# Optimization experiments

Hardware: AMD Instinct MI355X
Metric: run time of the kernel (lower is better)

Reference implementation:

```python
import jax, jax.numpy as jnp
import numpy as np

B, T, C, H = 4, 2048, 768, 12
D = C // H  # head dim = 64

def setup_inputs() -> dict:
    key = jax.random.key(0)
    k1, k2, k3 = jax.random.split(key, 3)
    x = jax.random.normal(k1, (B, T, C), dtype=jnp.float32)
    W_attn = jax.random.normal(k2, (C, 3 * C), dtype=jnp.float32) * 0.02
    b_attn = jnp.zeros((3 * C,), dtype=jnp.float32)
    W_proj = jax.random.normal(k3, (C, C), dtype=jnp.float32) * 0.02
    b_proj = jnp.zeros((C,), dtype=jnp.float32)
    return {"x": x, "W_attn": W_attn, "b_attn": b_attn, "W_proj": W_proj, "b_proj": b_proj}

def reference(x, W_attn, b_attn, W_proj, b_proj):
    Bx, Tx, Cx = x.shape
    qkv = x @ W_attn + b_attn                      # [B,T,3C]
    q, k, v = jnp.split(qkv, 3, axis=2)
    q = q.reshape(Bx, Tx, H, D).swapaxes(1, 2)     # [B,H,T,D]
    k = k.reshape(Bx, Tx, H, D).swapaxes(1, 2)
    v = v.reshape(Bx, Tx, H, D).swapaxes(1, 2)
    att = jnp.einsum('bhqd,bhkd->bhqk', q, k) / jnp.sqrt(jnp.float32(D))
    mask = jnp.tril(jnp.ones((Tx, Tx), dtype=bool))
    att = jnp.where(mask, att, -jnp.inf)
    att = jax.nn.softmax(att, axis=-1)
    y = jnp.einsum('bhqk,bhkd->bhqd', att, v)      # [B,H,T,D]
    y = y.swapaxes(1, 2).reshape(Bx, Tx, Cx)
    return y @ W_proj + b_proj
```

## Files before the change

### kernel.cpp

```cpp
#include <hip/hip_runtime.h>
#include <hip/hip_bf16.h>

#define BATCH 4
#define TSEQ  2048
#define CDIM  768
#define HNUM  12
#define DHEAD 64
#define NQKV  (3*CDIM)
#define BTOT  (BATCH*TSEQ)
#define BH    (BATCH*HNUM)

typedef unsigned short u16;
typedef __attribute__((ext_vector_type(8))) __bf16 bf16x8;
typedef __attribute__((ext_vector_type(4))) float f32x4;

#define MFMA16(a,b,c) __builtin_amdgcn_mfma_f32_16x16x32_bf16((a),(b),(c),0,0,0)

__device__ __forceinline__ u16 f2b(float f) {
    union { float f; unsigned u; } v; v.f = f;
    unsigned u = v.u;
    unsigned r = (u + 0x7fffu + ((u >> 16) & 1u)) >> 16;
    return (u16)r;
}

__device__ __forceinline__ unsigned cvtpk(float lo, float hi) {
    unsigned r;
    asm("v_cvt_pk_bf16_f32 %0, %1, %2" : "=v"(r) : "v"(lo), "v"(hi));
    return r;
}

__device__ __forceinline__ float fexp2(float x) {
    float r;
    asm("v_exp_f32 %0, %1" : "=v"(r) : "v"(x));
    return r;
}

__device__ __forceinline__ void gload_lds(const void* g, void* l) {
    __builtin_amdgcn_global_load_lds(
        (const __attribute__((address_space(1))) void*)g,
        (__attribute__((address_space(3))) void*)l, 16, 0, 0);
}

__global__ __launch_bounds__(256) void cast_f32_bf16(
        const float* __restrict__ in, u16* __restrict__ out, int n4) {
    int i = blockIdx.x * blockDim.x + threadIdx.x;
    if (i >= n4) return;
    float4 a = reinterpret_cast<const float4*>(in)[i];
    ushort4 o;
    o.x = f2b(a.x); o.y = f2b(a.y); o.z = f2b(a.z); o.w = f2b(a.w);
    reinterpret_cast<ushort4*>(out)[i] = o;
}

__global__ __launch_bounds__(256) void tcast(
        const float* __restrict__ in, u16* __restrict__ out, int R, int Cc) {
    __shared__ float tile[32][33];
    int c0 = blockIdx.x * 32, r0 = blockIdx.y * 32;
    int tx = threadIdx.x, ty = threadIdx.y;
    #pragma unroll
    for (int i = 0; i < 32; i += 8)
        tile[ty + i][tx] = in[(size_t)(r0 + ty + i) * Cc + c0 + tx];
    __syncthreads();
    #pragma unroll
    for (int i = 0; i < 32; i += 8)
        out[(size_t)(c0 + ty + i) * R + r0 + tx] = f2b(tile[tx][ty + i]);
}

template<int MODE>
__global__ __launch_bounds__(256) void gemm_bt(
        const u16* __restrict__ A, const u16* __restrict__ Bt,
        const float* __restrict__ bias,
        u16* __restrict__ qb, u16* __restrict__ kb, u16* __restrict__ vtb,
        float* __restrict__ outf, int M, int N, int K) {
    __shared__ u16 sA[2][128 * 32];
    __shared__ u16 sB[2][128 * 32];
    const int tid = threadIdx.x;
    const int lane = tid & 63;
    const int w = tid >> 6;
    const int wr = w >> 1, wc = w & 1;
    const int m0 = blockIdx.y * 128, n0 = blockIdx.x * 128;

    f32x4 acc[4][4] = {};

    auto stage = [&](int buf, int kt) {
        #pragma unroll
        for (int i = 0; i < 2; ++i) {
            int chunk = i * 256 + tid;
            int row = chunk >> 2, c8 = chunk & 3;
            gload_lds(A  + (size_t)(m0 + row) * K + kt * 32 + c8 * 8, &sA[buf][chunk * 8]);
            gload_lds(Bt + (size_t)(n0 + row) * K + kt * 32 + c8 * 8, &sB[buf][chunk * 8]);
        }
    };

    const int KT = K / 32;
    stage(0, 0);
    __syncthreads();
    for (int kt = 0; kt < KT; ++kt) {
        if (kt + 1 < KT) stage((kt + 1) & 1, kt + 1);
        const u16* cA = sA[kt & 1];
        const u16* cB = sB[kt & 1];
        bf16x8 af[4], bfr[4];
        #pragma unroll
        for (int m = 0; m < 4; ++m)
            af[m] = *(const bf16x8*)&cA[(wr * 64 + m * 16 + (lane & 15)) * 32 + ((lane >> 4) << 3)];
        #pragma unroll
        for (int n = 0; n < 4; ++n)
            bfr[n] = *(const bf16x8*)&cB[(wc * 64 + n * 16 + (lane & 15)) * 32 + ((lane >> 4) << 3)];
        #pragma unroll
        for (int m = 0; m < 4; ++m)
            #pragma unroll
            for (int n = 0; n < 4; ++n)
                acc[m][n] = MFMA16(af[m], bfr[n], acc[m][n]);
        __syncthreads();
    }

    if (MODE == 0) {
        const int which = n0 / CDIM;
        #pragma unroll
        for (int m = 0; m < 4; ++m) {
            #pragma unroll
            for (int n = 0; n < 4; ++n) {
                const int cg = n0 + wc * 64 + n * 16 + (lane & 15);
                const int c  = cg - which * CDIM;
                const int h  = c >> 6, d = c & 63;
                const float bv = bias[cg];
                const int rg0 = m0 + wr * 64 + m * 16 + ((lane >> 4) << 2);
                const int b = rg0 >> 11, t0 = rg0 & (TSEQ - 1);
                const size_t bh = (size_t)(b * HNUM + h);
                if (which == 2) {
                    ushort4 pv;
                    pv.x = f2b(acc[m][n][0] + bv);
                    pv.y = f2b(acc[m][n][1] + bv);
                    pv.z = f2b(acc[m][n][2] + bv);
                    pv.w = f2b(acc[m][n][3] + bv);
                    *(ushort4*)&vtb[(bh * DHEAD + d) * TSEQ + t0] = pv;
                } else {
                    #pragma unroll
                    for (int j = 0; j < 4; ++j) {
                        const float val = acc[m][n][j] + bv;
                        if (which == 0) qb[(bh * TSEQ + t0 + j) * DHEAD + d] = f2b(val * 0.1803368801111243f);
                        else            kb[(bh * TSEQ + t0 + j) * DHEAD + d] = f2b(val);
                    }
                }
            }
        }
    } else {
        #pragma unroll
        for (int m = 0; m < 4; ++m) {
            #pragma unroll
            for (int n = 0; n < 4; ++n) {
                const int cg = n0 + wc * 64 + n * 16 + (lane & 15);
                const float bv = bias[cg];
                #pragma unroll
                for (int j = 0; j < 4; ++j) {
                    const int rg = m0 + wr * 64 + m * 16 + ((lane >> 4) << 2) + j;
                    outf[(size_t)rg * CDIM + cg] = acc[m][n][j] + bv;
                }
            }
        }
    }
}

__global__ __launch_bounds__(512, 4) void attn_fwd(
        const u16* __restrict__ qb, const u16* __restrict__ kb,
        const u16* __restrict__ vtb, u16* __restrict__ yb) {
    __shared__ u16 sK[2][64 * 64];
    __shared__ u16 sVt[2][64 * 64];
    const int p  = blockIdx.x / BH;
    const int bh = blockIdx.x % BH;
    const int b = bh / HNUM, h = bh % HNUM;
    const int tid = threadIdx.x, lane = tid & 63, w = tid >> 6;
    const int g = lane >> 4, lq = lane & 15;
    const int qtile = (w < 4) ? p : (31 - p);
    const int qlo = qtile * 64 + (w & 3) * 16;
    const u16* qbase = qb  + (size_t)bh * TSEQ * DHEAD;
    const u16* kbase = kb  + (size_t)bh * TSEQ * DHEAD;
    const u16* vbase = vtb + (size_t)bh * DHEAD * TSEQ;

    bf16x8 qf[2];
    #pragma unroll
    for (int ks = 0; ks < 2; ++ks)
        qf[ks] = *(const bf16x8*)&qbase[(size_t)(qlo + lq) * DHEAD + ks * 32 + g * 8];

    f32x4 o[4] = {};
    float mx = -__builtin_inff(), ls = 0.f;

    const int srow = tid >> 3;
    const int lcol = (((tid & 7) << 4) ^ ((srow & 7) << 4)) >> 1;

    auto STAGE = [&](int buf, int kt) {
        const int k0 = kt << 6;
        gload_lds(kbase + (size_t)(k0 + srow) * DHEAD + lcol, &sK[buf][tid * 8]);
        gload_lds(vbase + (size_t)srow * TSEQ + k0 + lcol,    &sVt[buf][tid * 8]);
    };

    const int nk = 32 - p;
    STAGE(0, 0);
    __syncthreads();
    for (int kt = 0; kt < nk; ++kt) {
        const int k0 = kt << 6;
        if (kt + 1 < nk) STAGE((kt + 1) & 1, kt + 1);
        if (k0 <= qlo + 15) {
            const u16* cK = sK[kt & 1];
            const u16* cV = sVt[kt & 1];
            f32x4 s[4];
            #pragma unroll
            for (int n = 0; n < 4; ++n) s[n] = f32x4{0.f, 0.f, 0.f, 0.f};
            __builtin_amdgcn_s_setprio(1);
            #pragma unroll
            for (int n = 0; n < 4; ++n) {
                #pragma unroll
                for (int ks = 0; ks < 2; ++ks) {
                    int r = n * 16 + lq;
                    int lb = (r * 128 + (ks * 32 + g * 8) * 2) ^ ((r & 7) << 4);
                    bf16x8 kf = *(const bf16x8*)((const char*)cK + lb);
                    s[n] = MFMA16(kf, qf[ks], s[n]);
                }
            }
            __builtin_amdgcn_s_setprio(0);
            if (k0 + 63 > qlo) {
                const int qa = qlo + lq;
                #pragma unroll
                for (int n = 0; n < 4; ++n)
                    #pragma unroll
                    for (int j = 0; j < 4; ++j)
                        if (k0 + n * 16 + g * 4 + j > qa) s[n][j] = -__builtin_inff();
            }
            float t0 = fmaxf(fmaxf(s[0][0], s[0][1]), fmaxf(s[0][2], s[0][3]));
            float t1 = fmaxf(fmaxf(s[1][0], s[1][1]), fmaxf(s[1][2], s[1][3]));
            float t2 = fmaxf(fmaxf(s[2][0], s[2][1]), fmaxf(s[2][2], s[2][3]));
            float t3 = fmaxf(fmaxf(s[3][0], s[3][1]), fmaxf(s[3][2], s[3][3]));
            float tmax = fmaxf(fmaxf(t0, t1), fmaxf(t2, t3));
            tmax = fmaxf(tmax, __shfl_xor(tmax, 16));
            tmax = fmaxf(tmax, __shfl_xor(tmax, 32));
            if (__any(tmax > mx + 8.0f)) {
                float mnew = fmaxf(mx, tmax);
                float sc = fexp2(mx - mnew);
                mx = mnew;
                ls *= sc;
                #pragma unroll
                for (int j = 0; j < 4; ++j) {
                    float scj = __shfl(sc, (lane & 48) | ((g << 2) + j));
                    #pragma unroll
                    for (int n = 0; n < 4; ++n) o[n][j] *= scj;
                }
            }
            float rsum = 0.f;
            #pragma unroll
            for (int n = 0; n < 4; ++n)
                #pragma unroll
                for (int j = 0; j < 4; ++j) {
                    float pv = fexp2(s[n][j] - mx);
                    s[n][j] = pv;
                    rsum += pv;
                }
            rsum += __shfl_xor(rsum, 16);
            rsum += __shfl_xor(rsum, 32);
            ls += rsum;
            unsigned apk[4], bpk[4];
            #pragma unroll
            for (int n = 0; n < 4; ++n) {
                apk[n] = cvtpk(s[n][0], s[n][1]);
                bpk[n] = cvtpk(s[n][2], s[n][3]);
            }
            const int s0l = lq + ((lane & 16) << 1);
            const bool hi = (lane & 32) != 0;
            #pragma unroll
            for (int ks = 0; ks < 2; ++ks) {
                unsigned A0  = (unsigned)__shfl((int)apk[2 * ks],     s0l);
                unsigned B0  = (unsigned)__shfl((int)bpk[2 * ks],     s0l);
                unsigned A1  = (unsigned)__shfl((int)apk[2 * ks + 1], s0l);
                unsigned B1  = (unsigned)__shfl((int)bpk[2 * ks + 1], s0l);
                unsigned A0h = (unsigned)__shfl((int)apk[2 * ks],     s0l + 16);
                unsigned B0h = (unsigned)__shfl((int)bpk[2 * ks],     s0l + 16);
                unsigned A1h = (unsigned)__shfl((int)apk[2 * ks + 1], s0l + 16);
                unsigned B1h = (unsigned)__shfl((int)bpk[2 * ks + 1], s0l + 16);
                union { unsigned u[4]; bf16x8 v; } pa;
                pa.u[0] = hi ? A1  : A0;
                pa.u[1] = hi ? B1  : B0;
                pa.u[2] = hi ? A1h : A0h;
                pa.u[3] = hi ? B1h : B0h;
                __builtin_amdgcn_s_setprio(1);
                #pragma unroll
                for (int n = 0; n < 4; ++n) {
                    int d = n * 16 + lq;
                    int lb = (d * 128 + (ks * 32 + g * 8) * 2) ^ ((d & 7) << 4);
                    bf16x8 vf = *(const bf16x8*)((const char*)cV + lb);
                    o[n] = MFMA16(pa.v, vf, o[n]);
                }
                __builtin_amdgcn_s_setprio(0);
            }
        }
        __syncthreads();
    }

    #pragma unroll
    for (int j = 0; j < 4; ++j) {
        float lj = __shfl(ls, (lane & 48) | ((g << 2) + j));
        float inv = 1.f / lj;
        const int t = qlo + g * 4 + j;
        #pragma unroll
        for (int n = 0; n < 4; ++n) {
            const int c = h * DHEAD + n * 16 + lq;
            yb[((size_t)b * TSEQ + t) * CDIM + c] = f2b(o[n][j] * inv);
        }
    }
}

extern "C" void kernel_launch(void* const* d_in, const int* in_sizes, int n_in,
                              void* d_out, int out_size, void* d_ws, size_t ws_size,
                              hipStream_t stream) {
    const float* x      = (const float*)d_in[0];
    const float* W_attn = (const float*)d_in[1];
    const float* b_attn = (const float*)d_in[2];
    const float* W_proj = (const float*)d_in[3];
    const float* b_proj = (const float*)d_in[4];
    float* out = (float*)d_out;

    u16* ws = (u16*)d_ws;
    u16* xb     = ws;
    u16* yb     = xb;
    u16* WattnT = xb     + (size_t)BTOT * CDIM;
    u16* WprojT = WattnT + (size_t)NQKV * CDIM;
    u16* qb     = WprojT + (size_t)CDIM * CDIM;
    u16* kb     = qb     + (size_t)BH * TSEQ * DHEAD;
    u16* vtb    = kb     + (size_t)BH * TSEQ * DHEAD;

    int n4 = BTOT * CDIM / 4;
    cast_f32_bf16<<<(n4 + 255) / 256, 256, 0, stream>>>(x, xb, n4);
    tcast<<<dim3(NQKV / 32, CDIM / 32), dim3(32, 8), 0, stream>>>(W_attn, WattnT, CDIM, NQKV);
    tcast<<<dim3(CDIM / 32, CDIM / 32), dim3(32, 8), 0, stream>>>(W_proj, WprojT, CDIM, CDIM);

    gemm_bt<0><<<dim3(NQKV / 128, BTOT / 128), 256, 0, stream>>>(
        xb, WattnT, b_attn, qb, kb, vtb, nullptr, BTOT, NQKV, CDIM);

    attn_fwd<<<dim3((TSEQ / 128) * BH), 512, 0, stream>>>(qb, kb, vtb, yb);

    gemm_bt<1><<<dim3(CDIM / 128, BTOT / 128), 256, 0, stream>>>(
        yb, WprojT, b_proj, nullptr, nullptr, nullptr, out, BTOT, CDIM, CDIM);
}
```

Baseline: 166.9 us.

## Use one 64-row query tile per attention block and compute row sums via MFMA

Attention blocks shrink from 512 threads covering a paired short and long query tile to 256 threads covering a single 64-row tile. Blocks are ordered longest-first, and since the tile is diagonal-aligned every wave runs every key tile, so the per-wave causal skip branch is gone. The softmax denominator is now accumulated with an extra MFMA against a ones vector, replacing the shuffle reductions and the final broadcast. The cost is twice as many blocks, each staging two chunks per thread, and K/V tiles are no longer shared across two query tiles.

```diff
diff --git a/kernel.cpp b/kernel.cpp
--- a/kernel.cpp
+++ b/kernel.cpp
@@ -160,18 +160,17 @@
     }
 }
 
-__global__ __launch_bounds__(512, 4) void attn_fwd(
+__global__ __launch_bounds__(256, 4) void attn_fwd(
         const u16* __restrict__ qb, const u16* __restrict__ kb,
         const u16* __restrict__ vtb, u16* __restrict__ yb) {
     __shared__ u16 sK[2][64 * 64];
     __shared__ u16 sVt[2][64 * 64];
-    const int p  = blockIdx.x / BH;
+    const int qt = 31 - (int)(blockIdx.x / BH);
     const int bh = blockIdx.x % BH;
     const int b = bh / HNUM, h = bh % HNUM;
     const int tid = threadIdx.x, lane = tid & 63, w = tid >> 6;
     const int g = lane >> 4, lq = lane & 15;
-    const int qtile = (w < 4) ? p : (31 - p);
-    const int qlo = qtile * 64 + (w & 3) * 16;
+    const int qlo = qt * 64 + w * 16;
     const u16* qbase = qb  + (size_t)bh * TSEQ * DHEAD;
     const u16* kbase = kb  + (size_t)bh * TSEQ * DHEAD;
     const u16* vbase = vtb + (size_t)bh * DHEAD * TSEQ;
@@ -181,122 +180,121 @@
     for (int ks = 0; ks < 2; ++ks)
         qf[ks] = *(const bf16x8*)&qbase[(size_t)(qlo + lq) * DHEAD + ks * 32 + g * 8];
 
+    union { unsigned u[4]; bf16x8 v; } ones;
+    #pragma unroll
+    for (int i = 0; i < 4; ++i) ones.u[i] = 0x3f803f80u;
+
     f32x4 o[4] = {};
-    float mx = -__builtin_inff(), ls = 0.f;
-
-    const int srow = tid >> 3;
-    const int lcol = (((tid & 7) << 4) ^ ((srow & 7) << 4)) >> 1;
+    f32x4 ls = {};
+    float mx = -__builtin_inff();
 
     auto STAGE = [&](int buf, int kt) {
         const int k0 = kt << 6;
-        gload_lds(kbase + (size_t)(k0 + srow) * DHEAD + lcol, &sK[buf][tid * 8]);
-        gload_lds(vbase + (size_t)srow * TSEQ + k0 + lcol,    &sVt[buf][tid * 8]);
+        #pragma unroll
+        for (int i = 0; i < 2; ++i) {
+            int chunk = i * 256 + tid;
+            int srow = chunk >> 3;
+            int cb = ((chunk & 7) << 4) ^ ((srow & 7) << 4);
+            gload_lds(kbase + (size_t)(k0 + srow) * DHEAD + (cb >> 1), &sK[buf][chunk * 8]);
+            gload_lds(vbase + (size_t)srow * TSEQ + k0 + (cb >> 1),    &sVt[buf][chunk * 8]);
+        }
     };
 
-    const int nk = 32 - p;
+    const int nk = qt + 1;
     STAGE(0, 0);
     __syncthreads();
     for (int kt = 0; kt < nk; ++kt) {
         const int k0 = kt << 6;
         if (kt + 1 < nk) STAGE((kt + 1) & 1, kt + 1);
-        if (k0 <= qlo + 15) {
-            const u16* cK = sK[kt & 1];
-            const u16* cV = sVt[kt & 1];
-            f32x4 s[4];
-            #pragma unroll
-            for (int n = 0; n < 4; ++n) s[n] = f32x4{0.f, 0.f, 0.f, 0.f};
-            __builtin_amdgcn_s_setprio(1);
-            #pragma unroll
-            for (int n = 0; n < 4; ++n) {
-                #pragma unroll
-                for (int ks = 0; ks < 2; ++ks) {
-                    int r = n * 16 + lq;
-                    int lb = (r * 128 + (ks * 32 + g * 8) * 2) ^ ((r & 7) << 4);
-                    bf16x8 kf = *(const bf16x8*)((const char*)cK + lb);
-                    s[n] = MFMA16(kf, qf[ks], s[n]);
-                }
-            }
-            __builtin_amdgcn_s_setprio(0);
-            if (k0 + 63 > qlo) {
-                const int qa = qlo + lq;
-                #pragma unroll
-                for (int n = 0; n < 4; ++n)
-                    #pragma unroll
-                    for (int j = 0; j < 4; ++j)
-                        if (k0 + n * 16 + g * 4 + j > qa) s[n][j] = -__builtin_inff();
-            }
-            float t0 = fmaxf(fmaxf(s[0][0], s[0][1]), fmaxf(s[0][2], s[0][3]));
-            float t1 = fmaxf(fmaxf(s[1][0], s[1][1]), fmaxf(s[1][2], s[1][3]));
-            float t2 = fmaxf(fmaxf(s[2][0], s[2][1]), fmaxf(s[2][2], s[2][3]));
-            float t3 = fmaxf(fmaxf(s[3][0], s[3][1]), fmaxf(s[3][2], s[3][3]));
-            float tmax = fmaxf(fmaxf(t0, t1), fmaxf(t2, t3));
-            tmax = fmaxf(tmax, __shfl_xor(tmax, 16));
-            tmax = fmaxf(tmax, __shfl_xor(tmax, 32));
-            if (__any(tmax > mx + 8.0f)) {
-                float mnew = fmaxf(mx, tmax);
-                float sc = fexp2(mx - mnew);
-                mx = mnew;
-                ls *= sc;
-                #pragma unroll
-                for (int j = 0; j < 4; ++j) {
-                    float scj = __shfl(sc, (lane & 48) | ((g << 2) + j));
-                    #pragma unroll
-                    for (int n = 0; n < 4; ++n) o[n][j] *= scj;
-                }
-            }
-            float rsum = 0.f;
+        const u16* cK = sK[kt & 1];
+        const u16* cV = sVt[kt & 1];
+        f32x4 s[4];
+        #pragma unroll
+        for (int n = 0; n < 4; ++n) s[n] = f32x4{0.f, 0.f, 0.f, 0.f};
+        __builtin_amdgcn_s_setprio(1);
+        #pragma unroll
+        for (int n = 0; n < 4; ++n) {
+            #pragma unroll
+            for (int ks = 0; ks < 2; ++ks) {
+                int r = n * 16 + lq;
+                int lb = (r * 128 + (ks * 32 + g * 8) * 2) ^ ((r & 7) << 4);
+                bf16x8 kf = *(const bf16x8*)((const char*)cK + lb);
+                s[n] = MFMA16(kf, qf[ks], s[n]);
+            }
+        }
+        __builtin_amdgcn_s_setprio(0);
+        if (k0 + 63 > qlo) {
+            const int qa = qlo + lq;
             #pragma unroll
             for (int n = 0; n < 4; ++n)
                 #pragma unroll
-                for (int j = 0; j < 4; ++j) {
-                    float pv = fexp2(s[n][j] - mx);
-                    s[n][j] = pv;
-                    rsum += pv;
-                }
-            rsum += __shfl_xor(rsum, 16);
-            rsum += __shfl_xor(rsum, 32);
-            ls += rsum;
-            unsigned apk[4], bpk[4];
+                for (int j = 0; j < 4; ++j)
+                    if (k0 + n * 16 + g * 4 + j > qa) s[n][j] = -__builtin_inff();
+        }
+        float t0 = fmaxf(fmaxf(s[0][0], s[0][1]), fmaxf(s[0][2], s[0][3]));
+        float t1 = fmaxf(fmaxf(s[1][0], s[1][1]), fmaxf(s[1][2], s[1][3]));
+        float t2 = fmaxf(fmaxf(s[2][0], s[2][1]), fmaxf(s[2][2], s[2][3]));
+        float t3 = fmaxf(fmaxf(s[3][0], s[3][1]), fmaxf(s[3][2], s[3][3]));
+        float tmax = fmaxf(fmaxf(t0, t1), fmaxf(t2, t3));
+        tmax = fmaxf(tmax, __shfl_xor(tmax, 16));
+        tmax = fmaxf(tmax, __shfl_xor(tmax, 32));
+        if (__any(tmax > mx + 8.0f)) {
+            float mnew = fmaxf(mx, tmax);
+            float sc = fexp2(mx - mnew);
+            mx = mnew;
+            #pragma unroll
+            for (int j = 0; j < 4; ++j) {
+                float scj = __shfl(sc, (lane & 48) | ((g << 2) + j));
+                ls[j] *= scj;
+                #pragma unroll
+                for (int n = 0; n < 4; ++n) o[n][j] *= scj;
+            }
+        }
+        #pragma unroll
+        for (int n = 0; n < 4; ++n)
+            #pragma unroll
+            for (int j = 0; j < 4; ++j)
+                s[n][j] = fexp2(s[n][j] - mx);
+        unsigned apk[4], bpk[4];
+        #pragma unroll
+        for (int n = 0; n < 4; ++n) {
+            apk[n] = cvtpk(s[n][0], s[n][1]);
+            bpk[n] = cvtpk(s[n][2], s[n][3]);
+        }
+        const int s0l = lq + ((lane & 16) << 1);
+        const bool hi = (lane & 32) != 0;
+        #pragma unroll
+        for (int ks = 0; ks < 2; ++ks) {
+            unsigned A0  = (unsigned)__shfl((int)apk[2 * ks],     s0l);
+            unsigned B0  = (unsigned)__shfl((int)bpk[2 * ks],     s0l);
+            unsigned A1  = (unsigned)__shfl((int)apk[2 * ks + 1], s0l);
+            unsigned B1  = (unsigned)__shfl((int)bpk[2 * ks + 1], s0l);
+            unsigned A0h = (unsigned)__shfl((int)apk[2 * ks],     s0l + 16);
+            unsigned B0h = (unsigned)__shfl((int)bpk[2 * ks],     s0l + 16);
+            unsigned A1h = (unsigned)__shfl((int)apk[2 * ks + 1], s0l + 16);
+            unsigned B1h = (unsigned)__shfl((int)bpk[2 * ks + 1], s0l + 16);
+            union { unsigned u[4]; bf16x8 v; } pa;
+            pa.u[0] = hi ? A1  : A0;
+            pa.u[1] = hi ? B1  : B0;
+            pa.u[2] = hi ? A1h : A0h;
+            pa.u[3] = hi ? B1h : B0h;
+            __builtin_amdgcn_s_setprio(1);
             #pragma unroll
             for (int n = 0; n < 4; ++n) {
-                apk[n] = cvtpk(s[n][0], s[n][1]);
-                bpk[n] = cvtpk(s[n][2], s[n][3]);
-            }
-            const int s0l = lq + ((lane & 16) << 1);
-            const bool hi = (lane & 32) != 0;
-            #pragma unroll
-            for (int ks = 0; ks < 2; ++ks) {
-                unsigned A0  = (unsigned)__shfl((int)apk[2 * ks],     s0l);
-                unsigned B0  = (unsigned)__shfl((int)bpk[2 * ks],     s0l);
-                unsigned A1  = (unsigned)__shfl((int)apk[2 * ks + 1], s0l);
-                unsigned B1  = (unsigned)__shfl((int)bpk[2 * ks + 1], s0l);
-                unsigned A0h = (unsigned)__shfl((int)apk[2 * ks],     s0l + 16);
-                unsigned B0h = (unsigned)__shfl((int)bpk[2 * ks],     s0l + 16);
-                unsigned A1h = (unsigned)__shfl((int)apk[2 * ks + 1], s0l + 16);
-                unsigned B1h = (unsigned)__shfl((int)bpk[2 * ks + 1], s0l + 16);
-                union { unsigned u[4]; bf16x8 v; } pa;
-                pa.u[0] = hi ? A1  : A0;
-                pa.u[1] = hi ? B1  : B0;
-                pa.u[2] = hi ? A1h : A0h;
-                pa.u[3] = hi ? B1h : B0h;
-                __builtin_amdgcn_s_setprio(1);
-                #pragma unroll
-                for (int n = 0; n < 4; ++n) {
-                    int d = n * 16 + lq;
-                    int lb = (d * 128 + (ks * 32 + g * 8) * 2) ^ ((d & 7) << 4);
-                    bf16x8 vf = *(const bf16x8*)((const char*)cV + lb);
-                    o[n] = MFMA16(pa.v, vf, o[n]);
-                }
-                __builtin_amdgcn_s_setprio(0);
-            }
+                int d = n * 16 + lq;
+                int lb = (d * 128 + (ks * 32 + g * 8) * 2) ^ ((d & 7) << 4);
+                bf16x8 vf = *(const bf16x8*)((const char*)cV + lb);
+                o[n] = MFMA16(pa.v, vf, o[n]);
+            }
+            ls = MFMA16(pa.v, ones.v, ls);
+            __builtin_amdgcn_s_setprio(0);
         }
         __syncthreads();
     }
 
     #pragma unroll
     for (int j = 0; j < 4; ++j) {
-        float lj = __shfl(ls, (lane & 48) | ((g << 2) + j));
-        float inv = 1.f / lj;
+        float inv = 1.f / ls[j];
         const int t = qlo + g * 4 + j;
         #pragma unroll
         for (int n = 0; n < 4; ++n) {
@@ -333,7 +331,7 @@
     gemm_bt<0><<<dim3(NQKV / 128, BTOT / 128), 256, 0, stream>>>(
         xb, WattnT, b_attn, qb, kb, vtb, nullptr, BTOT, NQKV, CDIM);
 
-    attn_fwd<<<dim3((TSEQ / 128) * BH), 512, 0, stream>>>(qb, kb, vtb, yb);
+    attn_fwd<<<dim3((TSEQ / 64) * BH), 256, 0, stream>>>(qb, kb, vtb, yb);
 
     gemm_bt<1><<<dim3(CDIM / 128, BTOT / 128), 256, 0, stream>>>(
         yb, WprojT, b_proj, nullptr, nullptr, nullptr, out, BTOT, CDIM, CDIM);
```

Result: faster. 145.9 us (-12.6%).
